# Optimization experiments

Hardware: AMD Instinct MI355X
Metric: run time of the kernel (lower is better)

## Reference

```python
import jax, jax.numpy as jnp
import numpy as np

N = 20000      # nodes
E = 200000     # edges
IN = 128       # in_feat
OUT = 128      # out_feat
NB = 8         # num_bases
SI = IN // NB  # submat_in = 16
SO = OUT // NB # submat_out = 16
R = 230        # num_rels
T = 365        # total_times


def setup_inputs() -> dict:
    key = jax.random.key(0)
    ks = jax.random.split(key, 11)
    h = jax.random.normal(ks[0], (N, IN), jnp.float32)
    edge_norm = jax.random.uniform(ks[1], (E, 1), jnp.float32)
    node_norm = jax.random.uniform(ks[2], (N, 1), jnp.float32)
    weight = jax.random.normal(ks[3], (R, NB * SI * SO), jnp.float32) * 0.05
    h_bias = jnp.zeros((OUT,), jnp.float32)
    loop_weight = jax.random.normal(ks[4], (IN, OUT), jnp.float32) * 0.05
    time_embed = jax.random.normal(ks[5], (T, IN), jnp.float32) * 0.05
    edge_src = jax.random.randint(ks[6], (E,), 0, N)
    edge_dst = jax.random.randint(ks[7], (E,), 0, N)
    edge_type = jax.random.randint(ks[8], (E,), 0, R)
    time_idx = jax.random.randint(ks[9], (N,), 0, T)
    return dict(h=h, edge_norm=edge_norm, node_norm=node_norm, weight=weight,
                h_bias=h_bias, loop_weight=loop_weight, time_embed=time_embed,
                edge_src=edge_src, edge_dst=edge_dst, edge_type=edge_type,
                time_idx=time_idx)


def reference(h, edge_norm, node_norm, weight, h_bias, loop_weight, time_embed,
              edge_src, edge_dst, edge_type, time_idx):
    # self-loop message
    loop_message = h @ loop_weight                              # [N, OUT]
    # msg_func: per-edge relation weight gather + block-diagonal bmm
    W_e = weight[edge_type].reshape(-1, NB, SI, SO)             # [E, NB, SI, SO]
    src = h[edge_src].reshape(-1, NB, SI)                       # [E, NB, SI]
    msg = jnp.einsum('ebi,ebio->ebo', src, W_e).reshape(-1, OUT)  # [E, OUT]
    msg = msg * edge_norm
    # fn.sum aggregation over destination nodes
    agg = jax.ops.segment_sum(msg, edge_dst, num_segments=N)    # [N, OUT]
    # apply_func: scale by node norm, then bias + self loop + activation
    node_repr = agg * node_norm
    node_repr = node_repr + h_bias + loop_message
    node_repr = jax.nn.relu(node_repr)
    # get_time_embedding: per-node time embedding gather
    time_embedding = time_embed[time_idx]                       # [N, IN]
    return node_repr, time_embedding
```

## Files before the change

kernel.cpp:

```cpp
#include <hip/hip_runtime.h>

#define N 20000
#define E 200000
#define IN 128
#define OUT 128
#define NB 8
#define SI 16
#define SO 16
#define R 230
#define T 365

#define NSH 8
#define NSEG (R * NSH)

__device__ float  g_W_t[(size_t)R * NB * SO * SI];
__device__ ushort g_msg[(size_t)E * OUT];
__device__ int    g_cnt_d[N];
__device__ int    g_off_d[N];
__device__ int    g_cur_d[N];
__device__ int    g_cnt_r[NSEG * 16];
__device__ int    g_cur_r[NSEG * 16];
__device__ int    g_eid_r[E];
__device__ int    g_total_d;
__device__ int    g_total_r;

__device__ __forceinline__ ushort f2bf(float f) {
    unsigned u = __float_as_uint(f);
    return (ushort)((u + 0x7fffu + ((u >> 16) & 1u)) >> 16);
}
__device__ __forceinline__ float bflo(unsigned m) { return __uint_as_float(m << 16); }
__device__ __forceinline__ float bfhi(unsigned m) { return __uint_as_float(m & 0xffff0000u); }

__global__ __launch_bounds__(256) void hist_kernel(
        const float* __restrict__ weight,
        const int* __restrict__ edge_dst,
        const int* __restrict__ edge_type) {
    __shared__ int lh[NSEG];
    const int tid  = threadIdx.x;
    const int gtid = blockIdx.x * 256 + tid;
    const int GSZ  = gridDim.x * 256;

    for (int t = gtid; t < R * NB * SI * SO; t += GSZ) {
        int r  = t >> 11;
        int b  = (t >> 8) & 7;
        int ol = (t >> 4) & 15;
        int i  = t & 15;
        g_W_t[t] = weight[(long)r * 2048 + b * 256 + i * 16 + ol];
    }
    for (int j = tid; j < NSEG; j += 256) lh[j] = 0;
    __syncthreads();
    for (int e = gtid; e < E; e += GSZ) {
        atomicAdd(&g_cnt_d[edge_dst[e]], 1);
        atomicAdd(&lh[edge_type[e] * NSH + (e & (NSH - 1))], 1);
    }
    __syncthreads();
    for (int j = tid; j < NSEG; j += 256)
        if (lh[j]) atomicAdd(&g_cnt_r[j * 16], lh[j]);
}

__global__ __launch_bounds__(256) void alloc_kernel() {
    const int idx  = blockIdx.x * blockDim.x + threadIdx.x;
    const int lane = threadIdx.x & 63;
    const int NPAD = 20032;
    if (idx < NPAD) {
        int c = (idx < N) ? g_cnt_d[idx] : 0;
        int x = c;
        for (int d = 1; d < 64; d <<= 1) {
            int y = __shfl_up(x, d);
            if (lane >= d) x += y;
        }
        int base = 0;
        if (lane == 63) base = atomicAdd(&g_total_d, x);
        base = __shfl(base, 63);
        if (idx < N) {
            int off = base + x - c;
            g_off_d[idx] = off;
            g_cur_d[idx] = off;
        }
    } else {
        int j = idx - NPAD;
        if (j < 1856) {
            int c = (j < NSEG) ? g_cnt_r[j * 16] : 0;
            int x = c;
            for (int d = 1; d < 64; d <<= 1) {
                int y = __shfl_up(x, d);
                if (lane >= d) x += y;
            }
            int base = 0;
            if (lane == 63) base = atomicAdd(&g_total_r, x);
            base = __shfl(base, 63);
            if (j < NSEG) g_cur_r[j * 16] = base + x - c;
        }
    }
}

__global__ void scatter_kernel(const int* __restrict__ edge_type) {
    int e = blockIdx.x * blockDim.x + threadIdx.x;
    if (e < E) {
        int seg = edge_type[e] * NSH + (e & (NSH - 1));
        int pr = atomicAdd(&g_cur_r[seg * 16], 1);
        g_eid_r[pr] = e;
    }
}

__global__ __launch_bounds__(256) void msg_kernel(
        const float* __restrict__ h,
        const float* __restrict__ edge_norm,
        const int* __restrict__ edge_src,
        const int* __restrict__ edge_dst,
        const int* __restrict__ edge_type) {
    __shared__ __attribute__((aligned(16))) float hsm[32 * 132];
    __shared__ int   ssrc[32], stype[32], spos[32];
    __shared__ float snorm[32];

    const int tid = threadIdx.x;
    const int lo  = blockIdx.x * 32;

    if (tid < 32) {
        int e = g_eid_r[lo + tid];
        ssrc[tid]  = edge_src[e];
        stype[tid] = edge_type[e];
        snorm[tid] = edge_norm[e];
        spos[tid]  = atomicAdd(&g_cur_d[edge_dst[e]], 1);
    }
    __syncthreads();

    {
        const int row = tid >> 3;
        const int c0  = (tid & 7) * 4;
        const float* hp = h + (long)ssrc[row] * IN;
        float* dst = &hsm[row * 132];
#pragma unroll
        for (int j = 0; j < 4; ++j) {
            float4 v = *reinterpret_cast<const float4*>(hp + c0 + 32 * j);
            *reinterpret_cast<float4*>(dst + c0 + 32 * j) = v;
        }
    }
    __syncthreads();

    const int slot = tid >> 7;
    const int o    = tid & 127;
    const int b    = o >> 4;
    const int ol   = o & 15;

#define MSG_BODY(K, W0, W1, W2, W3)                                          \
    {                                                                        \
        const float* hrow = &hsm[(K) * 132 + b * 16];                        \
        float4 h0 = *reinterpret_cast<const float4*>(hrow);                  \
        float4 h1 = *reinterpret_cast<const float4*>(hrow + 4);              \
        float4 h2 = *reinterpret_cast<const float4*>(hrow + 8);              \
        float4 h3 = *reinterpret_cast<const float4*>(hrow + 12);             \
        float m0 = 0.f, m1 = 0.f;                                            \
        m0 = fmaf(h0.x, W0.x, m0); m0 = fmaf(h0.y, W0.y, m0);                \
        m0 = fmaf(h0.z, W0.z, m0); m0 = fmaf(h0.w, W0.w, m0);                \
        m1 = fmaf(h1.x, W1.x, m1); m1 = fmaf(h1.y, W1.y, m1);                \
        m1 = fmaf(h1.z, W1.z, m1); m1 = fmaf(h1.w, W1.w, m1);                \
        m0 = fmaf(h2.x, W2.x, m0); m0 = fmaf(h2.y, W2.y, m0);                \
        m0 = fmaf(h2.z, W2.z, m0); m0 = fmaf(h2.w, W2.w, m0);                \
        m1 = fmaf(h3.x, W3.x, m1); m1 = fmaf(h3.y, W3.y, m1);                \
        m1 = fmaf(h3.z, W3.z, m1); m1 = fmaf(h3.w, W3.w, m1);                \
        __builtin_nontemporal_store(f2bf(snorm[K] * (m0 + m1)),              \
                                    &g_msg[(long)spos[K] * OUT + o]);        \
    }

    if (stype[0] == stype[31]) {
        const float4* wp = reinterpret_cast<const float4*>(
            g_W_t + (long)stype[0] * 2048 + b * 256 + ol * 16);
        float4 w0 = wp[0], w1 = wp[1], w2 = wp[2], w3 = wp[3];
#pragma unroll 4
        for (int k = slot; k < 32; k += 2)
            MSG_BODY(k, w0, w1, w2, w3)
    } else {
        int rcur = -1;
        float4 w0, w1, w2, w3;
        for (int k = slot; k < 32; k += 2) {
            int r = stype[k];
            if (r != rcur) {
                const float4* wp = reinterpret_cast<const float4*>(
                    g_W_t + (long)r * 2048 + b * 256 + ol * 16);
                w0 = wp[0]; w1 = wp[1]; w2 = wp[2]; w3 = wp[3];
                rcur = r;
            }
            MSG_BODY(k, w0, w1, w2, w3)
        }
    }
#undef MSG_BODY
}

__global__ __launch_bounds__(256) void node_kernel(
        const float* __restrict__ h,
        const float* __restrict__ node_norm,
        const float* __restrict__ h_bias,
        const float* __restrict__ loop_weight,
        const float* __restrict__ time_embed,
        const int* __restrict__ time_idx,
        float* __restrict__ out) {
    const int t    = threadIdx.x;
    const int q    = t & 63;
    const int grp  = t >> 6;
    const int base = blockIdx.x * 16 + grp * 4;

    const unsigned* msg32 = reinterpret_cast<const unsigned*>(g_msg);

    float accL[4], accH[4];
#pragma unroll
    for (int nl = 0; nl < 4; ++nl) {
        const int n  = base + nl;
        const int st = g_off_d[n];
        const int cn = g_cnt_d[n];
        const unsigned* mp = msg32 + (size_t)st * 64 + q;
        float aL0 = 0.f, aL1 = 0.f, aH0 = 0.f, aH1 = 0.f;
        int k = 0;
        for (; k + 3 < cn; k += 4) {
            unsigned m0 = __builtin_nontemporal_load(mp + (size_t)(k + 0) * 64);
            unsigned m1 = __builtin_nontemporal_load(mp + (size_t)(k + 1) * 64);
            unsigned m2 = __builtin_nontemporal_load(mp + (size_t)(k + 2) * 64);
            unsigned m3 = __builtin_nontemporal_load(mp + (size_t)(k + 3) * 64);
            aL0 += bflo(m0); aH0 += bfhi(m0);
            aL1 += bflo(m1); aH1 += bfhi(m1);
            aL0 += bflo(m2); aH0 += bfhi(m2);
            aL1 += bflo(m3); aH1 += bfhi(m3);
        }
        for (; k < cn; ++k) {
            unsigned m = __builtin_nontemporal_load(mp + (size_t)k * 64);
            aL0 += bflo(m); aH0 += bfhi(m);
        }
        float nn = node_norm[n];
        accL[nl] = (aL0 + aL1) * nn;
        accH[nl] = (aH0 + aH1) * nn;
    }

    float slL0 = 0.f, slL1 = 0.f, slL2 = 0.f, slL3 = 0.f;
    float slH0 = 0.f, slH1 = 0.f, slH2 = 0.f, slH3 = 0.f;
    const float2* lw2 = reinterpret_cast<const float2*>(loop_weight);
    const float* hp0 = h + (size_t)(base + 0) * IN;
    const float* hp1 = h + (size_t)(base + 1) * IN;
    const float* hp2 = h + (size_t)(base + 2) * IN;
    const float* hp3 = h + (size_t)(base + 3) * IN;
#pragma unroll 4
    for (int i0 = 0; i0 < IN; i0 += 4) {
        float2 w0 = lw2[(size_t)(i0 + 0) * 64 + q];
        float2 w1 = lw2[(size_t)(i0 + 1) * 64 + q];
        float2 w2 = lw2[(size_t)(i0 + 2) * 64 + q];
        float2 w3 = lw2[(size_t)(i0 + 3) * 64 + q];
        float4 v0 = *reinterpret_cast<const float4*>(hp0 + i0);
        float4 v1 = *reinterpret_cast<const float4*>(hp1 + i0);
        float4 v2 = *reinterpret_cast<const float4*>(hp2 + i0);
        float4 v3 = *reinterpret_cast<const float4*>(hp3 + i0);
        slL0 = fmaf(v0.x, w0.x, slL0); slL0 = fmaf(v0.y, w1.x, slL0);
        slL0 = fmaf(v0.z, w2.x, slL0); slL0 = fmaf(v0.w, w3.x, slL0);
        slH0 = fmaf(v0.x, w0.y, slH0); slH0 = fmaf(v0.y, w1.y, slH0);
        slH0 = fmaf(v0.z, w2.y, slH0); slH0 = fmaf(v0.w, w3.y, slH0);
        slL1 = fmaf(v1.x, w0.x, slL1); slL1 = fmaf(v1.y, w1.x, slL1);
        slL1 = fmaf(v1.z, w2.x, slL1); slL1 = fmaf(v1.w, w3.x, slL1);
        slH1 = fmaf(v1.x, w0.y, slH1); slH1 = fmaf(v1.y, w1.y, slH1);
        slH1 = fmaf(v1.z, w2.y, slH1); slH1 = fmaf(v1.w, w3.y, slH1);
        slL2 = fmaf(v2.x, w0.x, slL2); slL2 = fmaf(v2.y, w1.x, slL2);
        slL2 = fmaf(v2.z, w2.x, slL2); slL2 = fmaf(v2.w, w3.x, slL2);
        slH2 = fmaf(v2.x, w0.y, slH2); slH2 = fmaf(v2.y, w1.y, slH2);
        slH2 = fmaf(v2.z, w2.y, slH2); slH2 = fmaf(v2.w, w3.y, slH2);
        slL3 = fmaf(v3.x, w0.x, slL3); slL3 = fmaf(v3.y, w1.x, slL3);
        slL3 = fmaf(v3.z, w2.x, slL3); slL3 = fmaf(v3.w, w3.x, slL3);
        slH3 = fmaf(v3.x, w0.y, slH3); slH3 = fmaf(v3.y, w1.y, slH3);
        slH3 = fmaf(v3.z, w2.y, slH3); slH3 = fmaf(v3.w, w3.y, slH3);
    }
    float slL[4] = {slL0, slL1, slL2, slL3};
    float slH[4] = {slH0, slH1, slH2, slH3};

    const float2 bias = reinterpret_cast<const float2*>(h_bias)[q];
    float2* o2  = reinterpret_cast<float2*>(out);
    float2* o2b = reinterpret_cast<float2*>(out + (size_t)N * OUT);
    const float2* te2 = reinterpret_cast<const float2*>(time_embed);
#pragma unroll
    for (int nl = 0; nl < 4; ++nl) {
        const int n = base + nl;
        float2 v;
        v.x = fmaxf(accL[nl] + bias.x + slL[nl], 0.f);
        v.y = fmaxf(accH[nl] + bias.y + slH[nl], 0.f);
        o2[(size_t)n * 64 + q] = v;
        o2b[(size_t)n * 64 + q] = te2[(size_t)time_idx[n] * 64 + q];
    }

    __syncthreads();
    if (t < 16) g_cnt_d[blockIdx.x * 16 + t] = 0;
    {
        int j = blockIdx.x * 256 + t;
        if (j < NSEG * 16) g_cnt_r[j] = 0;
    }
    if (blockIdx.x == 0 && t == 0) { g_total_d = 0; g_total_r = 0; }
}

extern "C" void kernel_launch(void* const* d_in, const int* in_sizes, int n_in,
                              void* d_out, int out_size, void* d_ws, size_t ws_size,
                              hipStream_t stream) {
    const float* h           = (const float*)d_in[0];
    const float* edge_norm   = (const float*)d_in[1];
    const float* node_norm   = (const float*)d_in[2];
    const float* weight      = (const float*)d_in[3];
    const float* h_bias      = (const float*)d_in[4];
    const float* loop_weight = (const float*)d_in[5];
    const float* time_embed  = (const float*)d_in[6];
    const int*   edge_src    = (const int*)d_in[7];
    const int*   edge_dst    = (const int*)d_in[8];
    const int*   edge_type   = (const int*)d_in[9];
    const int*   time_idx    = (const int*)d_in[10];
    float* out = (float*)d_out;

    hist_kernel<<<400, 256, 0, stream>>>(weight, edge_dst, edge_type);
    alloc_kernel<<<86, 256, 0, stream>>>();
    scatter_kernel<<<(E + 255) / 256, 256, 0, stream>>>(edge_type);
    msg_kernel<<<E / 32, 256, 0, stream>>>(h, edge_norm, edge_src,
                                           edge_dst, edge_type);
    node_kernel<<<N / 16, 256, 0, stream>>>(h, node_norm, h_bias, loop_weight,
                                            time_embed, time_idx, out);
}
```

Before: 222.1 us.

## Move self-loop GEMM and time-embedding gather into the alloc kernel

The self-loop matmul h @ loop_weight (plus bias) and the time-embedding gather move out of node_kernel into extra blocks of the formerly tiny alloc kernel, which used only 86 blocks. The self-loop result goes to a new global fp32 buffer g_sl that node_kernel reads back. The aim is to use the idle GPU while the prefix-scan runs and to slim the final node kernel. The cost is an extra 10 MB write and read of g_sl, and the alloc step, which sits on the critical path, becomes longer.

Result: no change. 219.1 us (-1.4%).

```diff
diff --git a/kernel.cpp b/kernel.cpp
--- a/kernel.cpp
+++ b/kernel.cpp
@@ -13,8 +13,14 @@
 #define NSH 8
 #define NSEG (R * NSH)
 
+#define ALLOC_BLOCKS 86
+#define SL_BLOCKS 625
+#define TE_BLOCKS 313
+#define GRID2 (ALLOC_BLOCKS + SL_BLOCKS + TE_BLOCKS)
+
 __device__ float  g_W_t[(size_t)R * NB * SO * SI];
 __device__ ushort g_msg[(size_t)E * OUT];
+__device__ float  g_sl[(size_t)N * OUT];
 __device__ int    g_cnt_d[N];
 __device__ int    g_off_d[N];
 __device__ int    g_cur_d[N];
@@ -45,7 +51,7 @@
         int b  = (t >> 8) & 7;
         int ol = (t >> 4) & 15;
         int i  = t & 15;
-        g_W_t[t] = weight[(long)r * 2048 + b * 256 + i * 16 + ol];
+        g_W_t[t] = weight[(size_t)r * 2048 + b * 256 + i * 16 + ol];
     }
     for (int j = tid; j < NSEG; j += 256) lh[j] = 0;
     __syncthreads();
@@ -58,39 +64,99 @@
         if (lh[j]) atomicAdd(&g_cnt_r[j * 16], lh[j]);
 }
 
-__global__ __launch_bounds__(256) void alloc_kernel() {
-    const int idx  = blockIdx.x * blockDim.x + threadIdx.x;
-    const int lane = threadIdx.x & 63;
-    const int NPAD = 20032;
-    if (idx < NPAD) {
-        int c = (idx < N) ? g_cnt_d[idx] : 0;
-        int x = c;
-        for (int d = 1; d < 64; d <<= 1) {
-            int y = __shfl_up(x, d);
-            if (lane >= d) x += y;
-        }
-        int base = 0;
-        if (lane == 63) base = atomicAdd(&g_total_d, x);
-        base = __shfl(base, 63);
-        if (idx < N) {
-            int off = base + x - c;
-            g_off_d[idx] = off;
-            g_cur_d[idx] = off;
-        }
-    } else {
-        int j = idx - NPAD;
-        if (j < 1856) {
-            int c = (j < NSEG) ? g_cnt_r[j * 16] : 0;
+__global__ __launch_bounds__(256) void alloc_aux_kernel(
+        const float* __restrict__ h,
+        const float* __restrict__ loop_weight,
+        const float* __restrict__ h_bias,
+        const float* __restrict__ time_embed,
+        const int* __restrict__ time_idx,
+        float* __restrict__ out) {
+    const int bid = blockIdx.x;
+    const int tid = threadIdx.x;
+
+    if (bid < ALLOC_BLOCKS) {
+        const int idx  = bid * 256 + tid;
+        const int lane = tid & 63;
+        const int NPAD = 20032;
+        if (idx < NPAD) {
+            int c = (idx < N) ? g_cnt_d[idx] : 0;
             int x = c;
             for (int d = 1; d < 64; d <<= 1) {
                 int y = __shfl_up(x, d);
                 if (lane >= d) x += y;
             }
             int base = 0;
-            if (lane == 63) base = atomicAdd(&g_total_r, x);
+            if (lane == 63) base = atomicAdd(&g_total_d, x);
             base = __shfl(base, 63);
-            if (j < NSEG) g_cur_r[j * 16] = base + x - c;
-        }
+            if (idx < N) {
+                int off = base + x - c;
+                g_off_d[idx] = off;
+                g_cur_d[idx] = off;
+            }
+        } else {
+            int j = idx - NPAD;
+            if (j < 1856) {
+                int c = (j < NSEG) ? g_cnt_r[j * 16] : 0;
+                int x = c;
+                for (int d = 1; d < 64; d <<= 1) {
+                    int y = __shfl_up(x, d);
+                    if (lane >= d) x += y;
+                }
+                int base = 0;
+                if (lane == 63) base = atomicAdd(&g_total_r, x);
+                base = __shfl(base, 63);
+                if (j < NSEG) g_cur_r[j * 16] = base + x - c;
+            }
+        }
+        return;
+    }
+
+    if (bid < ALLOC_BLOCKS + SL_BLOCKS) {
+        const int a    = bid - ALLOC_BLOCKS;
+        const int q    = tid & 63;
+        const int wave = tid >> 6;
+        const int nb   = a * 32 + wave * 8;
+        const float2* lw2 = reinterpret_cast<const float2*>(loop_weight);
+        float sL[8], sH[8];
+#pragma unroll
+        for (int j = 0; j < 8; ++j) { sL[j] = 0.f; sH[j] = 0.f; }
+        for (int i0 = 0; i0 < IN; i0 += 4) {
+            float2 w0 = lw2[(size_t)(i0 + 0) * 64 + q];
+            float2 w1 = lw2[(size_t)(i0 + 1) * 64 + q];
+            float2 w2 = lw2[(size_t)(i0 + 2) * 64 + q];
+            float2 w3 = lw2[(size_t)(i0 + 3) * 64 + q];
+#pragma unroll
+            for (int j = 0; j < 8; ++j) {
+                float4 v = *reinterpret_cast<const float4*>(
+                    h + (size_t)(nb + j) * IN + i0);
+                sL[j] = fmaf(v.x, w0.x, sL[j]); sL[j] = fmaf(v.y, w1.x, sL[j]);
+                sL[j] = fmaf(v.z, w2.x, sL[j]); sL[j] = fmaf(v.w, w3.x, sL[j]);
+                sH[j] = fmaf(v.x, w0.y, sH[j]); sH[j] = fmaf(v.y, w1.y, sH[j]);
+                sH[j] = fmaf(v.z, w2.y, sH[j]); sH[j] = fmaf(v.w, w3.y, sH[j]);
+            }
+        }
+        const float2 bias = reinterpret_cast<const float2*>(h_bias)[q];
+        float2* sl2 = reinterpret_cast<float2*>(g_sl);
+#pragma unroll
+        for (int j = 0; j < 8; ++j) {
+            float2 v; v.x = sL[j] + bias.x; v.y = sH[j] + bias.y;
+            sl2[(size_t)(nb + j) * 64 + q] = v;
+        }
+        return;
+    }
+
+    const int c    = bid - ALLOC_BLOCKS - SL_BLOCKS;
+    const int row  = tid >> 2;
+    const int part = tid & 3;
+    const int n    = c * 64 + row;
+    if (n < N) {
+        const float4* src = reinterpret_cast<const float4*>(
+            time_embed + (size_t)time_idx[n] * IN);
+        float4* dst = reinterpret_cast<float4*>(
+            out + (size_t)N * OUT + (size_t)n * IN);
+#pragma unroll
+        for (int j = 0; j < 8; ++j)
+            dst[part * 8 + j] = src[part * 8 + j];
     }
 }
 
@@ -128,7 +194,7 @@
     {
         const int row = tid >> 3;
         const int c0  = (tid & 7) * 4;
-        const float* hp = h + (long)ssrc[row] * IN;
+        const float* hp = h + (size_t)ssrc[row] * IN;
         float* dst = &hsm[row * 132];
 #pragma unroll
         for (int j = 0; j < 4; ++j) {
@@ -160,12 +226,12 @@
         m1 = fmaf(h3.x, W3.x, m1); m1 = fmaf(h3.y, W3.y, m1);                \
         m1 = fmaf(h3.z, W3.z, m1); m1 = fmaf(h3.w, W3.w, m1);                \
         __builtin_nontemporal_store(f2bf(snorm[K] * (m0 + m1)),              \
-                                    &g_msg[(long)spos[K] * OUT + o]);        \
+                                    &g_msg[(size_t)spos[K] * OUT + o]);      \
     }
 
     if (stype[0] == stype[31]) {
         const float4* wp = reinterpret_cast<const float4*>(
-            g_W_t + (long)stype[0] * 2048 + b * 256 + ol * 16);
+            g_W_t + (size_t)stype[0] * 2048 + b * 256 + ol * 16);
         float4 w0 = wp[0], w1 = wp[1], w2 = wp[2], w3 = wp[3];
 #pragma unroll 4
         for (int k = slot; k < 32; k += 2)
@@ -177,7 +243,7 @@
             int r = stype[k];
             if (r != rcur) {
                 const float4* wp = reinterpret_cast<const float4*>(
-                    g_W_t + (long)r * 2048 + b * 256 + ol * 16);
+                    g_W_t + (size_t)r * 2048 + b * 256 + ol * 16);
                 w0 = wp[0]; w1 = wp[1]; w2 = wp[2]; w3 = wp[3];
                 rcur = r;
             }
@@ -188,21 +254,17 @@
 }
 
 __global__ __launch_bounds__(256) void node_kernel(
-        const float* __restrict__ h,
         const float* __restrict__ node_norm,
-        const float* __restrict__ h_bias,
-        const float* __restrict__ loop_weight,
-        const float* __restrict__ time_embed,
-        const int* __restrict__ time_idx,
         float* __restrict__ out) {
     const int t    = threadIdx.x;
     const int q    = t & 63;
-    const int grp  = t >> 6;
-    const int base = blockIdx.x * 16 + grp * 4;
+    const int wave = t >> 6;
+    const int base = blockIdx.x * 16 + wave * 4;
 
     const unsigned* msg32 = reinterpret_cast<const unsigned*>(g_msg);
-
-    float accL[4], accH[4];
+    const float2*   sl2   = reinterpret_cast<const float2*>(g_sl);
+    float2*         o2    = reinterpret_cast<float2*>(out);
+
 #pragma unroll
     for (int nl = 0; nl < 4; ++nl) {
         const int n  = base + nl;
@@ -225,60 +287,12 @@
             unsigned m = __builtin_nontemporal_load(mp + (size_t)k * 64);
             aL0 += bflo(m); aH0 += bfhi(m);
         }
-        float nn = node_norm[n];
-        accL[nl] = (aL0 + aL1) * nn;
-        accH[nl] = (aH0 + aH1) * nn;
-    }
-
-    float slL0 = 0.f, slL1 = 0.f, slL2 = 0.f, slL3 = 0.f;
-    float slH0 = 0.f, slH1 = 0.f, slH2 = 0.f, slH3 = 0.f;
-    const float2* lw2 = reinterpret_cast<const float2*>(loop_weight);
-    const float* hp0 = h + (size_t)(base + 0) * IN;
-    const float* hp1 = h + (size_t)(base + 1) * IN;
-    const float* hp2 = h + (size_t)(base + 2) * IN;
-    const float* hp3 = h + (size_t)(base + 3) * IN;
-#pragma unroll 4
-    for (int i0 = 0; i0 < IN; i0 += 4) {
-        float2 w0 = lw2[(size_t)(i0 + 0) * 64 + q];
-        float2 w1 = lw2[(size_t)(i0 + 1) * 64 + q];
-        float2 w2 = lw2[(size_t)(i0 + 2) * 64 + q];
-        float2 w3 = lw2[(size_t)(i0 + 3) * 64 + q];
-        float4 v0 = *reinterpret_cast<const float4*>(hp0 + i0);
-        float4 v1 = *reinterpret_cast<const float4*>(hp1 + i0);
-        float4 v2 = *reinterpret_cast<const float4*>(hp2 + i0);
-        float4 v3 = *reinterpret_cast<const float4*>(hp3 + i0);
-        slL0 = fmaf(v0.x, w0.x, slL0); slL0 = fmaf(v0.y, w1.x, slL0);
-        slL0 = fmaf(v0.z, w2.x, slL0); slL0 = fmaf(v0.w, w3.x, slL0);
-        slH0 = fmaf(v0.x, w0.y, slH0); slH0 = fmaf(v0.y, w1.y, slH0);
-        slH0 = fmaf(v0.z, w2.y, slH0); slH0 = fmaf(v0.w, w3.y, slH0);
-        slL1 = fmaf(v1.x, w0.x, slL1); slL1 = fmaf(v1.y, w1.x, slL1);
-        slL1 = fmaf(v1.z, w2.x, slL1); slL1 = fmaf(v1.w, w3.x, slL1);
-        slH1 = fmaf(v1.x, w0.y, slH1); slH1 = fmaf(v1.y, w1.y, slH1);
-        slH1 = fmaf(v1.z, w2.y, slH1); slH1 = fmaf(v1.w, w3.y, slH1);
-        slL2 = fmaf(v2.x, w0.x, slL2); slL2 = fmaf(v2.y, w1.x, slL2);
-        slL2 = fmaf(v2.z, w2.x, slL2); slL2 = fmaf(v2.w, w3.x, slL2);
-        slH2 = fmaf(v2.x, w0.y, slH2); slH2 = fmaf(v2.y, w1.y, slH2);
-        slH2 = fmaf(v2.z, w2.y, slH2); slH2 = fmaf(v2.w, w3.y, slH2);
-        slL3 = fmaf(v3.x, w0.x, slL3); slL3 = fmaf(v3.y, w1.x, slL3);
-        slL3 = fmaf(v3.z, w2.x, slL3); slL3 = fmaf(v3.w, w3.x, slL3);
-        slH3 = fmaf(v3.x, w0.y, slH3); slH3 = fmaf(v3.y, w1.y, slH3);
-        slH3 = fmaf(v3.z, w2.y, slH3); slH3 = fmaf(v3.w, w3.y, slH3);
-    }
-    float slL[4] = {slL0, slL1, slL2, slL3};
-    float slH[4] = {slH0, slH1, slH2, slH3};
-
-    const float2 bias = reinterpret_cast<const float2*>(h_bias)[q];
-    float2* o2  = reinterpret_cast<float2*>(out);
-    float2* o2b = reinterpret_cast<float2*>(out + (size_t)N * OUT);
-    const float2* te2 = reinterpret_cast<const float2*>(time_embed);
-#pragma unroll
-    for (int nl = 0; nl < 4; ++nl) {
-        const int n = base + nl;
+        const float nn = node_norm[n];
+        const float2 sl = sl2[(size_t)n * 64 + q];
         float2 v;
-        v.x = fmaxf(accL[nl] + bias.x + slL[nl], 0.f);
-        v.y = fmaxf(accH[nl] + bias.y + slH[nl], 0.f);
+        v.x = fmaxf((aL0 + aL1) * nn + sl.x, 0.f);
+        v.y = fmaxf((aH0 + aH1) * nn + sl.y, 0.f);
         o2[(size_t)n * 64 + q] = v;
-        o2b[(size_t)n * 64 + q] = te2[(size_t)time_idx[n] * 64 + q];
     }
 
     __syncthreads();
@@ -307,10 +321,10 @@
     float* out = (float*)d_out;
 
     hist_kernel<<<400, 256, 0, stream>>>(weight, edge_dst, edge_type);
-    alloc_kernel<<<86, 256, 0, stream>>>();
+    alloc_aux_kernel<<<GRID2, 256, 0, stream>>>(h, loop_weight, h_bias,
+                                                time_embed, time_idx, out);
     scatter_kernel<<<(E + 255) / 256, 256, 0, stream>>>(edge_type);
     msg_kernel<<<E / 32, 256, 0, stream>>>(h, edge_norm, edge_src,
                                            edge_dst, edge_type);
-    node_kernel<<<N / 16, 256, 0, stream>>>(h, node_norm, h_bias, loop_weight,
-                                            time_embed, time_idx, out);
-}
+    node_kernel<<<N / 16, 256, 0, stream>>>(node_norm, out);
+}
```
